# Kernel tuning notes

Measured on AMD Instinct MI355X. Metric: run time of the kernel, lower is better.

## Reference

```python
import jax, jax.numpy as jnp
import numpy as np

N_EMBD = 768
N_HEAD = 12
HEAD_DIM = N_EMBD // N_HEAD


def setup_inputs() -> dict:
    key = jax.random.key(0)
    ks = jax.random.split(key, 5)
    B, T, C = 1, 4096, N_EMBD
    s = 1.0 / np.sqrt(C)
    return {
        "x": jax.random.normal(ks[0], (B, T, C), dtype=jnp.float32),
        "wq": jax.random.normal(ks[1], (C, C), dtype=jnp.float32) * s,
        "wk": jax.random.normal(ks[2], (C, C), dtype=jnp.float32) * s,
        "wv": jax.random.normal(ks[3], (C, C), dtype=jnp.float32) * s,
        "wo": jax.random.normal(ks[4], (C, C), dtype=jnp.float32) * s,
    }


def reference(x, wq, wk, wv, wo):
    B, T, C = x.shape
    H, D = N_HEAD, HEAD_DIM
    # projections: torch Linear(y = x @ W^T); weights stored as (out, in)
    q = (x @ wq.T).reshape(B, T, H, D).transpose(0, 2, 1, 3)  # B H T D
    k = (x @ wk.T).reshape(B, T, H, D).transpose(0, 2, 1, 3)
    v = (x @ wv.T).reshape(B, T, H, D).transpose(0, 2, 1, 3)
    scale = 1.0 / jnp.sqrt(jnp.asarray(D, dtype=x.dtype))
    attn = jnp.einsum("bhtd,bhsd->bhts", q, k) * scale  # B H T T
    causal = jnp.tril(jnp.ones((T, T), dtype=bool))
    attn = jnp.where(causal, attn, -jnp.inf)
    attn = jax.nn.softmax(attn, axis=-1)
    out = jnp.einsum("bhts,bhsd->bhtd", attn, v)  # B H T D
    out = out.transpose(0, 2, 1, 3).reshape(B, T, C)
    return out @ wo.T
```

## Files before the change

### kernel.cpp

```cpp
#include <hip/hip_runtime.h>


#define T_SEQ 4096
#define C_EMB 768
#define NH    12
#define HD    64

typedef __attribute__((ext_vector_type(8))) short bf16x8;
typedef __attribute__((ext_vector_type(4))) float floatx4;

#define QSCALE 0.18033688011112042f

__device__ __forceinline__ unsigned short f2bf(float f) {
  union { float f; unsigned u; } v; v.f = f;
  unsigned r = v.u + 0x7fffu + ((v.u >> 16) & 1u);
  return (unsigned short)(r >> 16);
}
__device__ __forceinline__ unsigned short f2bf_rhu(float f) {
  union { float f; unsigned u; } v; v.f = f;
  return (unsigned short)((v.u + 0x8000u) >> 16);
}
__device__ __forceinline__ float bf2f(unsigned short h) {
  union { unsigned u; float f; } v; v.u = ((unsigned)h) << 16;
  return v.f;
}

__device__ __forceinline__ void gload_lds16(const void* gptr, void* ldsptr) {
  __builtin_amdgcn_global_load_lds(
      (const __attribute__((address_space(1))) unsigned int*)gptr,
      (__attribute__((address_space(3))) unsigned int*)ldsptr,
      16, 0, 0);
}

__global__ void cast_all_kernel(const float* __restrict__ x,
                                const float* __restrict__ wq,
                                const float* __restrict__ wk,
                                const float* __restrict__ wv,
                                const float* __restrict__ wo,
                                unsigned short* __restrict__ dst) {
  const int GX = (T_SEQ * C_EMB) / 4;
  const int GW = (C_EMB * C_EMB) / 4;
  int i = blockIdx.x * blockDim.x + threadIdx.x;
  const float* src; int local;
  if (i < GX) { src = x; local = i; }
  else {
    int t = i - GX; int w = t / GW; local = t - w * GW;
    src = (w == 0) ? wq : (w == 1) ? wk : (w == 2) ? wv : wo;
  }
  float4 f = reinterpret_cast<const float4*>(src)[local];
  ushort4 u;
  u.x = f2bf(f.x); u.y = f2bf(f.y); u.z = f2bf(f.z); u.w = f2bf(f.w);
  reinterpret_cast<ushort4*>(dst)[i] = u;
}

__global__ __launch_bounds__(256) void gemm_qkv(
    const unsigned short* __restrict__ A,
    const unsigned short* __restrict__ B,
    unsigned short* __restrict__ Qb,
    unsigned short* __restrict__ Kb,
    unsigned short* __restrict__ Vt) {
  constexpr int K = 768, BM = 64, BN = 128, BK = 64;
  __shared__ __align__(16) unsigned short As[BM * BK];
  __shared__ __align__(16) unsigned short Bs[BN * BK];
  const int tid = threadIdx.x;
  const int wave = tid >> 6, lane = tid & 63;
  const int lm = lane & 15, lq = lane >> 4;
  const int swz = lm & 7;
  const int m0 = blockIdx.x * BM, n0 = blockIdx.y * BN;
  const int wm = (wave & 1) * 32, wn = (wave >> 1) * 64;
  floatx4 acc[2][4] = {};

  for (int k0 = 0; k0 < K; k0 += BK) {
#pragma unroll
    for (int i = 0; i < 2; i++) {
      int idx = i * 256 + tid;
      int row = idx >> 3;
      int ch = (idx & 7) ^ (row & 7);
      gload_lds16(A + (size_t)(m0 + row) * K + k0 + ch * 8, (char*)As + idx * 16);
    }
#pragma unroll
    for (int i = 0; i < 4; i++) {
      int idx = i * 256 + tid;
      int row = idx >> 3;
      int ch = (idx & 7) ^ (row & 7);
      gload_lds16(B + (size_t)(n0 + row) * K + k0 + ch * 8, (char*)Bs + idx * 16);
    }
    __syncthreads();
#pragma unroll
    for (int kk = 0; kk < 2; kk++) {
      bf16x8 af[2], bfr[4];
#pragma unroll
      for (int i = 0; i < 2; i++) {
        int row = wm + i * 16 + lm;
        af[i] = *(const bf16x8*)(As + row * BK + (((kk * 4 + lq) ^ swz) * 8));
      }
#pragma unroll
      for (int j = 0; j < 4; j++) {
        int row = wn + j * 16 + lm;
        bfr[j] = *(const bf16x8*)(Bs + row * BK + (((kk * 4 + lq) ^ swz) * 8));
      }
#pragma unroll
      for (int i = 0; i < 2; i++)
#pragma unroll
        for (int j = 0; j < 4; j++)
          acc[i][j] = __builtin_amdgcn_mfma_f32_16x16x32_bf16(af[i], bfr[j], acc[i][j], 0, 0, 0);
    }
    __syncthreads();
  }

  const int which = n0 / C_EMB;
  if (which < 2) {
    unsigned short* tgt = (which == 0) ? Qb : Kb;
    const float sc = (which == 0) ? QSCALE : 1.0f;
#pragma unroll
    for (int i = 0; i < 2; i++)
#pragma unroll
      for (int j = 0; j < 4; j++) {
        int n = n0 - which * C_EMB + wn + j * 16 + lm;
        int h = n >> 6, d = n & 63;
#pragma unroll
        for (int r = 0; r < 4; r++) {
          int m = m0 + wm + i * 16 + lq * 4 + r;
          tgt[(((size_t)h * T_SEQ + m) << 6) + d] = f2bf(acc[i][j][r] * sc);
        }
      }
  } else {
#pragma unroll
    for (int i = 0; i < 2; i++)
#pragma unroll
      for (int j = 0; j < 4; j++) {
        int n = n0 - 2 * C_EMB + wn + j * 16 + lm;
        int h = n >> 6, d = n & 63;
        int m = m0 + wm + i * 16 + lq * 4;
        ushort4 pk;
        pk.x = f2bf(acc[i][j][0]); pk.y = f2bf(acc[i][j][1]);
        pk.z = f2bf(acc[i][j][2]); pk.w = f2bf(acc[i][j][3]);
        *(ushort4*)(Vt + ((size_t)(h * HD + d)) * T_SEQ + m) = pk;
      }
  }
}

struct AttnState {
  float rsum[2][4];
  floatx4 o_acc[2][4];
};

template <typename EpilogueFn>
__device__ __forceinline__ void attn_body(
    const unsigned short* __restrict__ Q,
    const unsigned short* __restrict__ K,
    const unsigned short* __restrict__ Vt,
    int h, int q0, int sb, int se,
    unsigned short* Ks, unsigned short* Vs, unsigned short* Ps,
    EpilogueFn epi) {
  constexpr int BS = 64, PS = 72;
  const int tid = threadIdx.x;
  const int wave = tid >> 6, lane = tid & 63;
  const int lm = lane & 15, lq = lane >> 4;
  const unsigned short* Qh = Q + (size_t)h * T_SEQ * HD;
  const unsigned short* Kh = K + (size_t)h * T_SEQ * HD;
  const unsigned short* Vh = Vt + (size_t)h * HD * T_SEQ;
  const int qrow_base = q0 + wave * 32;
  unsigned short* Pw = Ps + wave * 32 * PS;
  const int swz = lm & 7;

  bf16x8 qf[2][2];
#pragma unroll
  for (int m = 0; m < 2; m++)
#pragma unroll
    for (int kk = 0; kk < 2; kk++)
      qf[m][kk] = *(const bf16x8*)(Qh + (size_t)(qrow_base + m * 16 + lm) * HD + kk * 32 + lq * 8);

  AttnState st;
#pragma unroll
  for (int m = 0; m < 2; m++)
#pragma unroll
    for (int r = 0; r < 4; r++) { st.rsum[m][r] = 0.f; st.o_acc[m][r] = floatx4{0.f,0.f,0.f,0.f}; }

  auto stage = [&](int s0) {
#pragma unroll
    for (int i = 0; i < 2; i++) {
      int idx = (wave * 2 + i) * 64 + lane;
      int row = idx >> 3;
      int ch = (idx & 7) ^ (row & 7);
      gload_lds16(Kh + (size_t)(s0 + row) * HD + ch * 8, (char*)Ks + idx * 16);
      gload_lds16(Vh + (size_t)row * T_SEQ + s0 + ch * 8, (char*)Vs + idx * 16);
    }
  };

  stage(sb * BS);
  for (int it = sb; it < se; ++it) {
    const int s0 = it * BS;
    __syncthreads();

    floatx4 sa[2][4] = {};
#pragma unroll
    for (int kk = 0; kk < 2; kk++)
#pragma unroll
      for (int j = 0; j < 4; j++) {
        int row = j * 16 + lm;
        bf16x8 kf = *(const bf16x8*)(Ks + (row * 8 + ((kk * 4 + lq) ^ swz)) * 8);
#pragma unroll
        for (int m = 0; m < 2; m++)
          sa[m][j] = __builtin_amdgcn_mfma_f32_16x16x32_bf16(qf[m][kk], kf, sa[m][j], 0, 0, 0);
      }

    if (s0 >= q0) {
#pragma unroll
      for (int m = 0; m < 2; m++)
#pragma unroll
        for (int j = 0; j < 4; j++) {
          int scol = s0 + j * 16 + lm;
#pragma unroll
          for (int r = 0; r < 4; r++) {
            int qrow = qrow_base + m * 16 + lq * 4 + r;
            if (scol > qrow) sa[m][j][r] = -1e30f;
          }
        }
    }

#pragma unroll
    for (int m = 0; m < 2; m++)
#pragma unroll
      for (int j = 0; j < 4; j++)
#pragma unroll
        for (int r = 0; r < 4; r++) {
          float p = __builtin_amdgcn_exp2f(sa[m][j][r]);
          st.rsum[m][r] += p;
          Pw[(m * 16 + lq * 4 + r) * PS + j * 16 + lm] = f2bf_rhu(p);
        }

#pragma unroll
    for (int kk = 0; kk < 2; kk++) {
      bf16x8 pf[2];
#pragma unroll
      for (int m = 0; m < 2; m++)
        pf[m] = *(const bf16x8*)(Pw + (m * 16 + lm) * PS + kk * 32 + lq * 8);
#pragma unroll
      for (int jd = 0; jd < 4; jd++) {
        int row = jd * 16 + lm;
        bf16x8 vf = *(const bf16x8*)(Vs + (row * 8 + ((kk * 4 + lq) ^ swz)) * 8);
#pragma unroll
        for (int m = 0; m < 2; m++)
          st.o_acc[m][jd] = __builtin_amdgcn_mfma_f32_16x16x32_bf16(pf[m], vf, st.o_acc[m][jd], 0, 0, 0);
      }
    }

    if (it + 1 < se) {
      __syncthreads();
      stage(s0 + BS);
    }
  }

#pragma unroll
  for (int m = 0; m < 2; m++)
#pragma unroll
    for (int r = 0; r < 4; r++) {
      float s = st.rsum[m][r];
      s += __shfl_xor(s, 1);
      s += __shfl_xor(s, 2);
      s += __shfl_xor(s, 4);
      s += __shfl_xor(s, 8);
      st.rsum[m][r] = s;
    }
  epi(st, qrow_base, lm, lq);
}

__global__ __launch_bounds__(256, 4) void attn_kernel2(
    const unsigned short* __restrict__ Q,
    const unsigned short* __restrict__ K,
    const unsigned short* __restrict__ Vt,
    unsigned short* __restrict__ Op0,
    unsigned short* __restrict__ Op1,
    float* __restrict__ lpart) {
  constexpr int BS = 64, PS = 72;
  __shared__ __align__(16) unsigned short Ks[BS * HD];
  __shared__ __align__(16) unsigned short Vs[HD * BS];
  __shared__ __align__(16) unsigned short Ps[4 * 32 * PS];
  const int bid = blockIdx.x;
  const int h = bid % NH;
  const int z = bid / NH;
  const int qt = (T_SEQ / 128 - 1) - (z >> 1);
  const int c = z & 1;
  const int q0 = qt * 128;
  const int sb = c ? (qt + 1) : 0;
  const int se = c ? (2 * qt + 2) : (qt + 1);

  unsigned short* Oc = c ? Op1 : Op0;
  float* lc = lpart + (size_t)c * NH * T_SEQ;
  attn_body(Q, K, Vt, h, q0, sb, se, Ks, Vs, Ps,
    [&](const AttnState& st, int qrow_base, int lm, int lq) {
#pragma unroll
      for (int m = 0; m < 2; m++)
#pragma unroll
        for (int r = 0; r < 4; r++) {
          int t = qrow_base + m * 16 + lq * 4 + r;
          if (lm == 0) lc[h * T_SEQ + t] = st.rsum[m][r];
#pragma unroll
          for (int jd = 0; jd < 4; jd++)
            Oc[((size_t)h * T_SEQ + t) * HD + jd * 16 + lm] = f2bf(st.o_acc[m][jd][r]);
        }
    });
}

__global__ void combine_kernel2(const unsigned short* __restrict__ Op0,
                                const unsigned short* __restrict__ Op1,
                                const float* __restrict__ lpart,
                                unsigned short* __restrict__ Ob) {
  int idx = blockIdx.x * blockDim.x + threadIdx.x;
  int d4 = idx & 15;
  int t = (idx >> 4) & (T_SEQ - 1);
  int h = idx >> 16;
  float l = lpart[h * T_SEQ + t] + lpart[NH * T_SEQ + h * T_SEQ + t];
  float inv = 1.0f / l;
  ushort4 a = reinterpret_cast<const ushort4*>(Op0)[idx];
  ushort4 b = reinterpret_cast<const ushort4*>(Op1)[idx];
  ushort4 u;
  u.x = f2bf((bf2f(a.x) + bf2f(b.x)) * inv);
  u.y = f2bf((bf2f(a.y) + bf2f(b.y)) * inv);
  u.z = f2bf((bf2f(a.z) + bf2f(b.z)) * inv);
  u.w = f2bf((bf2f(a.w) + bf2f(b.w)) * inv);
  *(ushort4*)(Ob + (size_t)t * C_EMB + h * HD + d4 * 4) = u;
}

__global__ __launch_bounds__(256, 4) void attn_kernel4(
    const unsigned short* __restrict__ Q,
    const unsigned short* __restrict__ K,
    const unsigned short* __restrict__ Vt,
    float* __restrict__ Opart,
    float* __restrict__ lpart) {
  constexpr int BS = 64, PS = 72;
  __shared__ __align__(16) unsigned short Ks[BS * HD];
  __shared__ __align__(16) unsigned short Vs[HD * BS];
  __shared__ __align__(16) unsigned short Ps[4 * 32 * PS];
  const int bid = blockIdx.x;
  const int h = bid % NH;
  const int z = bid / NH;
  const int qt = (T_SEQ / 128 - 1) - (z >> 2);
  const int c = z & 3;
  const int q0 = qt * 128;
  const int n = 2 * qt + 2;
  const int sb = (n * c) >> 2, se = (n * (c + 1)) >> 2;
  if (sb == se) return;

  const size_t CN = (size_t)NH * T_SEQ * HD;
  float* Oc = Opart + (size_t)c * CN;
  float* lc = lpart + (size_t)c * NH * T_SEQ;
  attn_body(Q, K, Vt, h, q0, sb, se, Ks, Vs, Ps,
    [&](const AttnState& st, int qrow_base, int lm, int lq) {
#pragma unroll
      for (int m = 0; m < 2; m++)
#pragma unroll
        for (int r = 0; r < 4; r++) {
          int t = qrow_base + m * 16 + lq * 4 + r;
          if (lm == 0) lc[h * T_SEQ + t] = st.rsum[m][r];
#pragma unroll
          for (int jd = 0; jd < 4; jd++)
            Oc[((size_t)h * T_SEQ + t) * HD + jd * 16 + lm] = st.o_acc[m][jd][r];
        }
    });
}

__global__ void combine_kernel4(const float* __restrict__ Opart,
                                const float* __restrict__ lpart,
                                unsigned short* __restrict__ Ob) {
  int idx = blockIdx.x * blockDim.x + threadIdx.x;
  int d4 = idx & 15;
  int t = (idx >> 4) & (T_SEQ - 1);
  int h = idx >> 16;
  const int qt = t >> 7;
  const int n = 2 * qt + 2;
  const size_t CN4 = (size_t)NH * T_SEQ * HD / 4;
  float4 o = make_float4(0.f, 0.f, 0.f, 0.f);
  float l = 0.f;
#pragma unroll
  for (int c = 0; c < 4; c++) {
    if (((n * c) >> 2) != ((n * (c + 1)) >> 2)) {
      float4 p = reinterpret_cast<const float4*>(Opart)[c * CN4 + idx];
      o.x += p.x; o.y += p.y; o.z += p.z; o.w += p.w;
      l += lpart[c * NH * T_SEQ + h * T_SEQ + t];
    }
  }
  float inv = 1.0f / l;
  ushort4 u;
  u.x = f2bf(o.x * inv); u.y = f2bf(o.y * inv);
  u.z = f2bf(o.z * inv); u.w = f2bf(o.w * inv);
  *(ushort4*)(Ob + (size_t)t * C_EMB + h * HD + d4 * 4) = u;
}

__global__ __launch_bounds__(256) void gemm_out(
    const unsigned short* __restrict__ A,
    const unsigned short* __restrict__ B,
    float* __restrict__ Out) {
  constexpr int K = 768, BM = 64, BN = 128, BK = 64;
  __shared__ __align__(16) unsigned short As[BM * BK];
  __shared__ __align__(16) unsigned short Bs[BN * BK];
  const int tid = threadIdx.x;
  const int wave = tid >> 6, lane = tid & 63;
  const int lm = lane & 15, lq = lane >> 4;
  const int swz = lm & 7;
  const int m0 = blockIdx.x * BM, n0 = blockIdx.y * BN;
  const int wm = (wave & 1) * 32, wn = (wave >> 1) * 64;
  floatx4 acc[2][4] = {};

  for (int k0 = 0; k0 < K; k0 += BK) {
#pragma unroll
    for (int i = 0; i < 2; i++) {
      int idx = i * 256 + tid;
      int row = idx >> 3;
      int ch = (idx & 7) ^ (row & 7);
      gload_lds16(A + (size_t)(m0 + row) * K + k0 + ch * 8, (char*)As + idx * 16);
    }
#pragma unroll
    for (int i = 0; i < 4; i++) {
      int idx = i * 256 + tid;
      int row = idx >> 3;
      int ch = (idx & 7) ^ (row & 7);
      gload_lds16(B + (size_t)(n0 + row) * K + k0 + ch * 8, (char*)Bs + idx * 16);
    }
    __syncthreads();
#pragma unroll
    for (int kk = 0; kk < 2; kk++) {
      bf16x8 af[2], bfr[4];
#pragma unroll
      for (int i = 0; i < 2; i++) {
        int row = wm + i * 16 + lm;
        af[i] = *(const bf16x8*)(As + row * BK + (((kk * 4 + lq) ^ swz) * 8));
      }
#pragma unroll
      for (int j = 0; j < 4; j++) {
        int row = wn + j * 16 + lm;
        bfr[j] = *(const bf16x8*)(Bs + row * BK + (((kk * 4 + lq) ^ swz) * 8));
      }
#pragma unroll
      for (int i = 0; i < 2; i++)
#pragma unroll
        for (int j = 0; j < 4; j++)
          acc[i][j] = __builtin_amdgcn_mfma_f32_16x16x32_bf16(af[i], bfr[j], acc[i][j], 0, 0, 0);
    }
    __syncthreads();
  }
#pragma unroll
  for (int i = 0; i < 2; i++)
#pragma unroll
    for (int j = 0; j < 4; j++)
#pragma unroll
      for (int r = 0; r < 4; r++) {
        int m = m0 + wm + i * 16 + lq * 4 + r;
        int n = n0 + wn + j * 16 + lm;
        Out[(size_t)m * C_EMB + n] = acc[i][j][r];
      }
}

extern "C" void kernel_launch(void* const* d_in, const int* in_sizes, int n_in,
                              void* d_out, int out_size, void* d_ws, size_t ws_size,
                              hipStream_t stream) {
  const float* x  = (const float*)d_in[0];
  const float* wq = (const float*)d_in[1];
  const float* wk = (const float*)d_in[2];
  const float* wv = (const float*)d_in[3];
  const float* wo = (const float*)d_in[4];
  float* out = (float*)d_out;

  const size_t XN = (size_t)T_SEQ * C_EMB;
  const size_t WN = (size_t)C_EMB * C_EMB;
  unsigned short* base = (unsigned short*)d_ws;

  unsigned short* Xb   = base;
  unsigned short* Wqkv = base + XN;
  unsigned short* Wob  = base + XN + 3 * WN;
  unsigned short* Qb   = base + XN + 4 * WN;
  unsigned short* Kb   = Qb + XN;
  unsigned short* Vt   = Kb + XN;
  unsigned short* tail = Vt + XN;
  unsigned short* Ob   = Qb;

  const size_t needA = 29884416ull + 4ull * XN * 4ull + 4ull * NH * T_SEQ * 4ull;

  const int ngroups = (int)((XN + 4 * WN) / 4);
  cast_all_kernel<<<dim3(ngroups / 256), 256, 0, stream>>>(x, wq, wk, wv, wo, Xb);

  gemm_qkv<<<dim3(T_SEQ / 64, 2304 / 128), 256, 0, stream>>>(Xb, Wqkv, Qb, Kb, Vt);

  if (ws_size >= needA) {
    float* Opart4 = (float*)tail;
    float* lpart4 = Opart4 + 4 * XN;
    attn_kernel4<<<dim3((T_SEQ / 128) * 4 * NH), 256, 0, stream>>>(Qb, Kb, Vt, Opart4, lpart4);
    combine_kernel4<<<dim3((int)(XN / 4) / 256), 256, 0, stream>>>(Opart4, lpart4, Ob);
  } else {
    unsigned short* Op0 = base;
    unsigned short* Op1 = tail;
    float* lpart = (float*)(base + XN);
    attn_kernel2<<<dim3((T_SEQ / 128) * 2 * NH), 256, 0, stream>>>(Qb, Kb, Vt, Op0, Op1, lpart);
    combine_kernel2<<<dim3((int)(XN / 4) / 256), 256, 0, stream>>>(Op0, Op1, lpart, Ob);
  }

  gemm_out<<<dim3(T_SEQ / 64, C_EMB / 128), 256, 0, stream>>>(Ob, Wob, out);
}
```

Before: 166.2 us.

## Load K/V fragments directly from global into registers, dropping LDS staging

The attention body no longer stages K and V tiles into shared memory via async global-to-LDS copies. Each wave now reads its K and V MFMA fragments straight from global memory (relying on L2/L1 caching) and does not synchronise. This removes the block-wide barriers and the LDS traffic. In exchange, the four waves each read the same K/V tile redundantly, and the loads no longer overlap with compute through prefetch. The extra fragment registers lead to lowering the occupancy hint from 4 to 3 blocks per CU.

```diff
diff --git a/kernel.cpp b/kernel.cpp
--- a/kernel.cpp
+++ b/kernel.cpp
@@ -151,7 +151,7 @@
     const unsigned short* __restrict__ K,
     const unsigned short* __restrict__ Vt,
     int h, int q0, int sb, int se,
-    unsigned short* Ks, unsigned short* Vs, unsigned short* Ps,
+    unsigned short* Ps,
     EpilogueFn epi) {
   constexpr int BS = 64, PS = 72;
   const int tid = threadIdx.x;
@@ -162,7 +162,6 @@
   const unsigned short* Vh = Vt + (size_t)h * HD * T_SEQ;
   const int qrow_base = q0 + wave * 32;
   unsigned short* Pw = Ps + wave * 32 * PS;
-  const int swz = lm & 7;
 
   bf16x8 qf[2][2];
 #pragma unroll
@@ -177,33 +176,31 @@
 #pragma unroll
     for (int r = 0; r < 4; r++) { st.rsum[m][r] = 0.f; st.o_acc[m][r] = floatx4{0.f,0.f,0.f,0.f}; }
 
-  auto stage = [&](int s0) {
-#pragma unroll
-    for (int i = 0; i < 2; i++) {
-      int idx = (wave * 2 + i) * 64 + lane;
-      int row = idx >> 3;
-      int ch = (idx & 7) ^ (row & 7);
-      gload_lds16(Kh + (size_t)(s0 + row) * HD + ch * 8, (char*)Ks + idx * 16);
-      gload_lds16(Vh + (size_t)row * T_SEQ + s0 + ch * 8, (char*)Vs + idx * 16);
-    }
-  };
-
-  stage(sb * BS);
   for (int it = sb; it < se; ++it) {
     const int s0 = it * BS;
-    __syncthreads();
+
+    bf16x8 kf[2][4];
+#pragma unroll
+    for (int kk = 0; kk < 2; kk++)
+#pragma unroll
+      for (int j = 0; j < 4; j++)
+        kf[kk][j] = *(const bf16x8*)(Kh + (size_t)(s0 + j * 16 + lm) * HD + (kk * 4 + lq) * 8);
 
     floatx4 sa[2][4] = {};
 #pragma unroll
     for (int kk = 0; kk < 2; kk++)
 #pragma unroll
-      for (int j = 0; j < 4; j++) {
-        int row = j * 16 + lm;
-        bf16x8 kf = *(const bf16x8*)(Ks + (row * 8 + ((kk * 4 + lq) ^ swz)) * 8);
+      for (int j = 0; j < 4; j++)
 #pragma unroll
         for (int m = 0; m < 2; m++)
-          sa[m][j] = __builtin_amdgcn_mfma_f32_16x16x32_bf16(qf[m][kk], kf, sa[m][j], 0, 0, 0);
-      }
+          sa[m][j] = __builtin_amdgcn_mfma_f32_16x16x32_bf16(qf[m][kk], kf[kk][j], sa[m][j], 0, 0, 0);
+
+    bf16x8 vf[2][4];
+#pragma unroll
+    for (int kk = 0; kk < 2; kk++)
+#pragma unroll
+      for (int jd = 0; jd < 4; jd++)
+        vf[kk][jd] = *(const bf16x8*)(Vh + (size_t)(jd * 16 + lm) * T_SEQ + s0 + (kk * 4 + lq) * 8);
 
     if (s0 >= q0) {
 #pragma unroll
@@ -237,18 +234,10 @@
       for (int m = 0; m < 2; m++)
         pf[m] = *(const bf16x8*)(Pw + (m * 16 + lm) * PS + kk * 32 + lq * 8);
 #pragma unroll
-      for (int jd = 0; jd < 4; jd++) {
-        int row = jd * 16 + lm;
-        bf16x8 vf = *(const bf16x8*)(Vs + (row * 8 + ((kk * 4 + lq) ^ swz)) * 8);
+      for (int jd = 0; jd < 4; jd++)
 #pragma unroll
         for (int m = 0; m < 2; m++)
-          st.o_acc[m][jd] = __builtin_amdgcn_mfma_f32_16x16x32_bf16(pf[m], vf, st.o_acc[m][jd], 0, 0, 0);
-      }
-    }
-
-    if (it + 1 < se) {
-      __syncthreads();
-      stage(s0 + BS);
+          st.o_acc[m][jd] = __builtin_amdgcn_mfma_f32_16x16x32_bf16(pf[m], vf[kk][jd], st.o_acc[m][jd], 0, 0, 0);
     }
   }
 
@@ -266,16 +255,14 @@
   epi(st, qrow_base, lm, lq);
 }
 
-__global__ __launch_bounds__(256, 4) void attn_kernel2(
+__global__ __launch_bounds__(256, 3) void attn_kernel2(
     const unsigned short* __restrict__ Q,
     const unsigned short* __restrict__ K,
     const unsigned short* __restrict__ Vt,
     unsigned short* __restrict__ Op0,
     unsigned short* __restrict__ Op1,
     float* __restrict__ lpart) {
-  constexpr int BS = 64, PS = 72;
-  __shared__ __align__(16) unsigned short Ks[BS * HD];
-  __shared__ __align__(16) unsigned short Vs[HD * BS];
+  constexpr int PS = 72;
   __shared__ __align__(16) unsigned short Ps[4 * 32 * PS];
   const int bid = blockIdx.x;
   const int h = bid % NH;
@@ -288,7 +275,7 @@
 
   unsigned short* Oc = c ? Op1 : Op0;
   float* lc = lpart + (size_t)c * NH * T_SEQ;
-  attn_body(Q, K, Vt, h, q0, sb, se, Ks, Vs, Ps,
+  attn_body(Q, K, Vt, h, q0, sb, se, Ps,
     [&](const AttnState& st, int qrow_base, int lm, int lq) {
 #pragma unroll
       for (int m = 0; m < 2; m++)
@@ -323,15 +310,13 @@
   *(ushort4*)(Ob + (size_t)t * C_EMB + h * HD + d4 * 4) = u;
 }
 
-__global__ __launch_bounds__(256, 4) void attn_kernel4(
+__global__ __launch_bounds__(256, 3) void attn_kernel4(
     const unsigned short* __restrict__ Q,
     const unsigned short* __restrict__ K,
     const unsigned short* __restrict__ Vt,
     float* __restrict__ Opart,
     float* __restrict__ lpart) {
-  constexpr int BS = 64, PS = 72;
-  __shared__ __align__(16) unsigned short Ks[BS * HD];
-  __shared__ __align__(16) unsigned short Vs[HD * BS];
+  constexpr int PS = 72;
   __shared__ __align__(16) unsigned short Ps[4 * 32 * PS];
   const int bid = blockIdx.x;
   const int h = bid % NH;
@@ -346,7 +331,7 @@
   const size_t CN = (size_t)NH * T_SEQ * HD;
   float* Oc = Opart + (size_t)c * CN;
   float* lc = lpart + (size_t)c * NH * T_SEQ;
-  attn_body(Q, K, Vt, h, q0, sb, se, Ks, Vs, Ps,
+  attn_body(Q, K, Vt, h, q0, sb, se, Ps,
     [&](const AttnState& st, int qrow_base, int lm, int lq) {
 #pragma unroll
       for (int m = 0; m < 2; m++)
```

New measurement: 228.1 us. +37.2%, slower.
